# Kernel tuning notes

Hardware: AMD Instinct MI355X
Metric: run time of the kernel (lower is better)

## Reference

```python
import jax, jax.numpy as jnp
import numpy as np

D_MODEL = 1024
HEADS = 16
HEAD_DIM = D_MODEL // HEADS
FF = 4 * D_MODEL
EPS = 1e-5


def _layer_norm(x, g, b):
    mu = jnp.mean(x, axis=-1, keepdims=True)
    var = jnp.mean(jnp.square(x - mu), axis=-1, keepdims=True)
    return (x - mu) * jax.lax.rsqrt(var + EPS) * g + b


def setup_inputs() -> dict:
    key = jax.random.key(0)
    ks = jax.random.split(key, 12)
    s = 0.02
    inp = {
        "x": jax.random.normal(ks[0], (2, 2048, D_MODEL), dtype=jnp.float32),
        "Wq": jax.random.normal(ks[1], (D_MODEL, D_MODEL), dtype=jnp.float32) * s,
        "bq": jnp.zeros((D_MODEL,), jnp.float32),
        "Wk": jax.random.normal(ks[2], (D_MODEL, D_MODEL), dtype=jnp.float32) * s,
        "bk": jnp.zeros((D_MODEL,), jnp.float32),
        "Wv": jax.random.normal(ks[3], (D_MODEL, D_MODEL), dtype=jnp.float32) * s,
        "bv": jnp.zeros((D_MODEL,), jnp.float32),
        "Wm": jax.random.normal(ks[4], (D_MODEL, D_MODEL), dtype=jnp.float32) * s,
        "bm": jnp.zeros((D_MODEL,), jnp.float32),
        "W1": jax.random.normal(ks[5], (D_MODEL, FF), dtype=jnp.float32) * s,
        "b1": jnp.zeros((FF,), jnp.float32),
        "W2": jax.random.normal(ks[6], (FF, D_MODEL), dtype=jnp.float32) * s,
        "b2": jnp.zeros((D_MODEL,), jnp.float32),
        "g1": jnp.ones((D_MODEL,), jnp.float32),
        "be1": jnp.zeros((D_MODEL,), jnp.float32),
        "g2": jnp.ones((D_MODEL,), jnp.float32),
        "be2": jnp.zeros((D_MODEL,), jnp.float32),
    }
    return inp


def reference(x, Wq, bq, Wk, bk, Wv, bv, Wm, bm, W1, b1, W2, b2, g1, be1, g2, be2):
    B, L, _ = x.shape
    # self-attention: source = x, no pos, no masks
    q = (x @ Wq + bq).reshape(B, L, HEADS, HEAD_DIM).transpose(0, 2, 1, 3)
    k = (x @ Wk + bk).reshape(B, L, HEADS, HEAD_DIM).transpose(0, 2, 1, 3)
    v = (x @ Wv + bv).reshape(B, L, HEADS, HEAD_DIM).transpose(0, 2, 1, 3)
    scale = 1.0 / np.sqrt(HEAD_DIM).astype(np.float32)
    scores = jnp.einsum("bhld,bhsd->bhls", q, k) * scale  # [B,H,L,L]
    attn = jax.nn.softmax(scores, axis=-1)
    msg = jnp.einsum("bhls,bhsd->bhld", attn, v)
    msg = msg.transpose(0, 2, 1, 3).reshape(B, L, D_MODEL)
    msg = msg @ Wm + bm
    h = _layer_norm(x + msg, g1, be1)
    ffn = jax.nn.relu(h @ W1 + b1) @ W2 + b2
    return _layer_norm(h + ffn, g2, be2)
```

## Files before the change

### kernel.cpp

```cpp
#include <hip/hip_runtime.h>

#define D_MODEL 1024
#define N_TOK   4096
#define HEADS   16
#define FF_DIM  4096
#define SEQ_L   2048

typedef unsigned short u16;
typedef unsigned int   u32;
typedef __bf16 bf16x8 __attribute__((ext_vector_type(8)));
typedef float  f32x4  __attribute__((ext_vector_type(4)));

#define AS1C(p) ((const __attribute__((address_space(1))) void*)(p))
#define AS3(p)  ((__attribute__((address_space(3))) void*)(p))

__device__ __forceinline__ u16 f2bf(float f) {
    union { float f; unsigned u; } c; c.f = f;
    return (u16)((c.u + 0x7fffu + ((c.u >> 16) & 1u)) >> 16);
}
__device__ __forceinline__ float bf2f(u16 b) {
    union { unsigned u; float f; } c; c.u = ((unsigned)b) << 16;
    return c.f;
}
__device__ __forceinline__ u32 cvt_pk_bf16(float lo, float hi) {
    u32 r;
    asm("v_cvt_pk_bf16_f32 %0, %1, %2" : "=v"(r) : "v"(lo), "v"(hi));
    return r;
}
__device__ __forceinline__ float fmax3(float a, float b, float c) {
    float r;
    asm("v_max3_f32 %0, %1, %2, %3" : "=v"(r) : "v"(a), "v"(b), "v"(c));
    return r;
}

template<int RELU>
__global__ __launch_bounds__(512, 2)
void gemm_pipe(const u16* __restrict__ A, const u16* __restrict__ Bt,
               const float* __restrict__ bias, u16* __restrict__ C,
               int M, int N, int K)
{
    __shared__ u16 As[2][256 * 64];
    __shared__ u16 Bs[2][256 * 64];

    const int tid = threadIdx.x;
    const int wid = tid >> 6, lane = tid & 63;
    const int wr  = wid >> 2, wc = wid & 3;
    const int l15 = lane & 15, l16 = lane >> 4;

    const int nwg = gridDim.x * gridDim.y;
    int bid = blockIdx.y * gridDim.x + blockIdx.x;
    bid = (bid & 7) * (nwg >> 3) + (bid >> 3);
    const int r0 = (bid / gridDim.x) * 256, c0 = (bid % gridDim.x) * 256;

    const u16* Ab = A  + (size_t)r0 * K;
    const u16* Bb = Bt + (size_t)c0 * K;

    f32x4 acc[8][4];
#pragma unroll
    for (int m = 0; m < 8; ++m)
#pragma unroll
        for (int n = 0; n < 4; ++n) acc[m][n] = (f32x4){0.f, 0.f, 0.f, 0.f};

    auto stage = [&](u16* dst, const u16* src, int kbase) {
#pragma unroll
        for (int i = 0; i < 4; ++i) {
            const int r  = i * 64 + (tid >> 3);
            const int gc = (tid & 7) ^ (r & 7);
            __builtin_amdgcn_global_load_lds(AS1C(src + (size_t)r * K + kbase + gc * 8),
                                             AS3(dst + (i * 64 + (wid << 3)) * 64), 16, 0, 0);
        }
    };

    bf16x8 af[4][2], bbA[2][2], bbB[2][2];

    auto ldAf = [&](const u16* sl, int mh) {
#pragma unroll
        for (int m = 0; m < 4; ++m) {
            const int row = wr * 128 + (mh * 4 + m) * 16 + l15;
#pragma unroll
            for (int ks = 0; ks < 2; ++ks) {
                const int ch = (ks * 4 + l16) ^ (row & 7);
                af[m][ks] = *(const bf16x8*)&sl[row * 64 + ch * 8];
            }
        }
    };
    auto ldBf = [&](const u16* sl, int pair, bf16x8 (&bb)[2][2]) {
#pragma unroll
        for (int n = 0; n < 2; ++n) {
            const int row = wc * 64 + (pair * 2 + n) * 16 + l15;
#pragma unroll
            for (int ks = 0; ks < 2; ++ks) {
                const int ch = (ks * 4 + l16) ^ (row & 7);
                bb[n][ks] = *(const bf16x8*)&sl[row * 64 + ch * 8];
            }
        }
    };
    auto mm16 = [&](int mh, int pair, bf16x8 (&bb)[2][2]) {
        __builtin_amdgcn_s_setprio(1);
#pragma unroll
        for (int ks = 0; ks < 2; ++ks)
#pragma unroll
            for (int m = 0; m < 4; ++m)
#pragma unroll
                for (int n = 0; n < 2; ++n)
                    acc[mh * 4 + m][pair * 2 + n] =
                        __builtin_amdgcn_mfma_f32_16x16x32_bf16(af[m][ks], bb[n][ks],
                                                                acc[mh * 4 + m][pair * 2 + n], 0, 0, 0);
        __builtin_amdgcn_s_setprio(0);
    };

    const int nt = K >> 6;
    stage(&As[0][0], Ab, 0);
    stage(&Bs[0][0], Bb, 0);
    stage(&As[1][0], Ab, 64);

    for (int t = 0; t < nt; ++t) {
        u16* Asl = &As[t & 1][0];
        u16* Bsl = &Bs[t & 1][0];
        u16* Aso = &As[t & 1][0];
        u16* Bso = &Bs[(t + 1) & 1][0];

        if (t + 1 < nt) { asm volatile("s_waitcnt vmcnt(4)" ::: "memory"); }
        else            { asm volatile("s_waitcnt vmcnt(0)" ::: "memory"); }
        __builtin_amdgcn_s_barrier();
        ldAf(Asl, 0);
        ldBf(Bsl, 0, bbA);
        if (t + 1 < nt) stage(Bso, Bb, (t + 1) * 64);
        __builtin_amdgcn_s_barrier();
        mm16(0, 0, bbA);
        __builtin_amdgcn_s_barrier();
        ldBf(Bsl, 1, bbB);
        mm16(0, 1, bbB);
        __builtin_amdgcn_s_barrier();
        ldAf(Asl, 1);
        mm16(1, 0, bbA);
        __builtin_amdgcn_s_barrier();
        if (t + 2 < nt) stage(Aso, Ab, (t + 2) * 64);
        mm16(1, 1, bbB);
        __builtin_amdgcn_s_barrier();
    }

#pragma unroll
    for (int n = 0; n < 4; ++n) {
        const int col = c0 + wc * 64 + n * 16 + l15;
        const float bv = bias[col];
#pragma unroll
        for (int m = 0; m < 8; ++m) {
#pragma unroll
            for (int r = 0; r < 4; ++r) {
                const size_t row = (size_t)(r0 + wr * 128 + m * 16 + l16 * 4 + r);
                float v = acc[m][n][r] + bv;
                if (RELU) v = fmaxf(v, 0.f);
                C[row * N + col] = f2bf(v);
            }
        }
    }
}

template<int RELU>
__global__ __launch_bounds__(512, 2)
void gemm_pipe128(const u16* __restrict__ A, const u16* __restrict__ Bt,
                  const float* __restrict__ bias, u16* __restrict__ C,
                  int M, int N, int K)
{
    __shared__ u16 As[2][128 * 64];
    __shared__ u16 Bs[2][128 * 64];

    const int tid = threadIdx.x;
    const int wid = tid >> 6, lane = tid & 63;
    const int wr  = wid >> 2, wc = wid & 3;
    const int l15 = lane & 15, l16 = lane >> 4;

    const int nwg = gridDim.x * gridDim.y;
    int bid = blockIdx.y * gridDim.x + blockIdx.x;
    bid = (bid & 7) * (nwg >> 3) + (bid >> 3);
    const int r0 = (bid / gridDim.x) * 128, c0 = (bid % gridDim.x) * 128;

    const u16* Ab = A  + (size_t)r0 * K;
    const u16* Bb = Bt + (size_t)c0 * K;

    f32x4 acc[4][2];
#pragma unroll
    for (int m = 0; m < 4; ++m)
#pragma unroll
        for (int n = 0; n < 2; ++n) acc[m][n] = (f32x4){0.f, 0.f, 0.f, 0.f};

    auto stage = [&](u16* dst, const u16* src, int kbase) {
#pragma unroll
        for (int i = 0; i < 2; ++i) {
            const int r  = i * 64 + (tid >> 3);
            const int gc = (tid & 7) ^ (r & 7);
            __builtin_amdgcn_global_load_lds(AS1C(src + (size_t)r * K + kbase + gc * 8),
                                             AS3(dst + (i * 64 + (wid << 3)) * 64), 16, 0, 0);
        }
    };

    const int nt = K >> 6;
    stage(&As[0][0], Ab, 0);  stage(&Bs[0][0], Bb, 0);
    stage(&As[1][0], Ab, 64); stage(&Bs[1][0], Bb, 64);

    for (int t = 0; t < nt; ++t) {
        const u16* Asl = &As[t & 1][0];
        const u16* Bsl = &Bs[t & 1][0];

        if (t + 1 < nt) { asm volatile("s_waitcnt vmcnt(4)" ::: "memory"); }
        else            { asm volatile("s_waitcnt vmcnt(0)" ::: "memory"); }
        __builtin_amdgcn_s_barrier();

        bf16x8 af[4][2], bb[2][2];
#pragma unroll
        for (int m = 0; m < 4; ++m) {
            const int row = wr * 64 + m * 16 + l15;
#pragma unroll
            for (int ks = 0; ks < 2; ++ks) {
                const int ch = (ks * 4 + l16) ^ (row & 7);
                af[m][ks] = *(const bf16x8*)&Asl[row * 64 + ch * 8];
            }
        }
#pragma unroll
        for (int n = 0; n < 2; ++n) {
            const int row = wc * 32 + n * 16 + l15;
#pragma unroll
            for (int ks = 0; ks < 2; ++ks) {
                const int ch = (ks * 4 + l16) ^ (row & 7);
                bb[n][ks] = *(const bf16x8*)&Bsl[row * 64 + ch * 8];
            }
        }
        __builtin_amdgcn_s_setprio(1);
#pragma unroll
        for (int ks = 0; ks < 2; ++ks)
#pragma unroll
            for (int m = 0; m < 4; ++m)
#pragma unroll
                for (int n = 0; n < 2; ++n)
                    acc[m][n] = __builtin_amdgcn_mfma_f32_16x16x32_bf16(af[m][ks], bb[n][ks], acc[m][n], 0, 0, 0);
        __builtin_amdgcn_s_setprio(0);
        __builtin_amdgcn_s_barrier();

        if (t + 2 < nt) {
            stage(&As[t & 1][0], Ab, (t + 2) * 64);
            stage(&Bs[t & 1][0], Bb, (t + 2) * 64);
        }
    }

#pragma unroll
    for (int n = 0; n < 2; ++n) {
        const int col = c0 + wc * 32 + n * 16 + l15;
        const float bv = bias[col];
#pragma unroll
        for (int m = 0; m < 4; ++m) {
#pragma unroll
            for (int r = 0; r < 4; ++r) {
                const size_t row = (size_t)(r0 + wr * 64 + m * 16 + l16 * 4 + r);
                float v = acc[m][n][r] + bv;
                if (RELU) v = fmaxf(v, 0.f);
                C[row * N + col] = f2bf(v);
            }
        }
    }
}

__global__ __launch_bounds__(512, 4)
void attn_mfma(const u16* __restrict__ qkv, u16* __restrict__ ao)
{
    __shared__ u16 Kl[2][128 * 64];
    __shared__ u32 Vt[64 * 64];

    const int tid = threadIdx.x;
    const int wid = tid >> 6, lane = tid & 63;
    const int l15 = lane & 15, l16 = lane >> 4;

    int lin = blockIdx.y * gridDim.x + blockIdx.x;
    lin = (lin & 7) * 64 + (lin >> 3);
    const int bh = lin >> 4, b = bh >> 4, h = bh & 15;
    const int q0 = (lin & 15) * 128;
    const int ho = h * 64;
    const size_t tb = (size_t)b * SEQ_L;

    const u16* qg = qkv + (tb + q0) * 3072 + ho;
    const u16* kg = qkv + tb * 3072 + 1024 + ho;
    const u16* vg = qkv + tb * 3072 + 2048 + ho;

    const float SC = 0.18033688f;

    bf16x8 qa[2];
#pragma unroll
    for (int ks = 0; ks < 2; ++ks) {
        union { bf16x8 v; u16 u[8]; u32 w[4]; } a, r;
        a.v = *(const bf16x8*)(qg + (size_t)(wid * 16 + l15) * 3072 + ks * 32 + l16 * 8);
#pragma unroll
        for (int e = 0; e < 4; ++e)
            r.w[e] = cvt_pk_bf16(bf2f(a.u[2 * e]) * SC, bf2f(a.u[2 * e + 1]) * SC);
        qa[ks] = r.v;
    }

    union { bf16x8 v; u32 u[4]; } onesv;
#pragma unroll
    for (int e = 0; e < 4; ++e) onesv.u[e] = 0x3F803F80u;

    const int sp = lane;
    const int dc = wid;

    auto stageK = [&](int buf, int s0) {
#pragma unroll
        for (int i = 0; i < 2; ++i) {
            const int r  = i * 64 + (tid >> 3);
            const int gc = (tid & 7) ^ (r & 7);
            __builtin_amdgcn_global_load_lds(AS1C(kg + (size_t)(s0 + r) * 3072 + gc * 8),
                                             AS3(&Kl[buf][(i * 64 + wid * 8) * 64]), 16, 0, 0);
        }
    };

    f32x4 oacc[4];
#pragma unroll
    for (int f = 0; f < 4; ++f) oacc[f] = (f32x4){0.f, 0.f, 0.f, 0.f};
    f32x4 lcol = (f32x4){0.f, 0.f, 0.f, 0.f};
    float m_c = -1e30f;

    union { bf16x8 v; u16 u[8]; } ua, ub;
    stageK(0, 0);
    ua.v = *(const bf16x8*)(vg + (size_t)(2 * sp) * 3072 + dc * 8);
    ub.v = *(const bf16x8*)(vg + (size_t)(2 * sp + 1) * 3072 + dc * 8);

    const int nt = SEQ_L / 128;
    for (int t = 0; t < nt; ++t) {
        const int buf = t & 1;

        asm volatile("s_waitcnt vmcnt(0)" ::: "memory");
#pragma unroll
        for (int e = 0; e < 8; ++e) {
            const int d = dc * 8 + e;
            const int w = sp ^ (((d & 7) << 2) ^ ((d >> 3) << 1));
            Vt[d * 64 + w] = (u32)ua.u[e] | ((u32)ub.u[e] << 16);
        }
        __syncthreads();

        if (t + 1 < nt) {
            stageK(buf ^ 1, (t + 1) * 128);
            ua.v = *(const bf16x8*)(vg + (size_t)((t + 1) * 128 + 2 * sp) * 3072 + dc * 8);
            ub.v = *(const bf16x8*)(vg + (size_t)((t + 1) * 128 + 2 * sp + 1) * 3072 + dc * 8);
        }

        f32x4 sacc[8];
#pragma unroll
        for (int f = 0; f < 8; ++f) sacc[f] = (f32x4){0.f, 0.f, 0.f, 0.f};
        __builtin_amdgcn_s_setprio(1);
#pragma unroll
        for (int ks = 0; ks < 2; ++ks)
#pragma unroll
            for (int f = 0; f < 8; ++f) {
                const int row = f * 16 + l15;
                const int ch  = (ks * 4 + l16) ^ (row & 7);
                bf16x8 kb = *(const bf16x8*)&Kl[buf][row * 64 + ch * 8];
                sacc[f] = __builtin_amdgcn_mfma_f32_16x16x32_bf16(kb, qa[ks], sacc[f], 0, 0, 0);
            }
        __builtin_amdgcn_s_setprio(0);

        float pm[8];
#pragma unroll
        for (int f = 0; f < 8; ++f)
            pm[f] = fmaxf(fmax3(sacc[f][0], sacc[f][1], sacc[f][2]), sacc[f][3]);
        float mx;
        {
            float t0 = fmax3(pm[0], pm[1], pm[2]);
            float t1 = fmax3(pm[3], pm[4], pm[5]);
            float t2 = fmaxf(pm[6], pm[7]);
            mx = fmax3(t0, t1, t2);
        }
        mx = fmaxf(mx, __shfl_xor(mx, 16));
        mx = fmaxf(mx, __shfl_xor(mx, 32));

        if (__any(mx > m_c + 8.f)) {
            const float mnew = fmaxf(m_c, mx);
            const float corr = __builtin_exp2f(m_c - mnew);
            m_c = mnew;
#pragma unroll
            for (int r = 0; r < 4; ++r) {
                const float cr = __shfl(corr, l16 * 4 + r);
                lcol[r] *= cr;
#pragma unroll
                for (int f = 0; f < 4; ++f) oacc[f][r] *= cr;
            }
        }

#pragma unroll
        for (int f = 0; f < 8; ++f)
#pragma unroll
            for (int r = 0; r < 4; ++r)
                sacc[f][r] = __builtin_exp2f(sacc[f][r] - m_c);

        u32 pk[8][2];
#pragma unroll
        for (int f = 0; f < 8; ++f) {
            pk[f][0] = cvt_pk_bf16(sacc[f][0], sacc[f][1]);
            pk[f][1] = cvt_pk_bf16(sacc[f][2], sacc[f][3]);
        }

        __builtin_amdgcn_s_setprio(1);
#pragma unroll
        for (int S = 0; S < 4; ++S) {
            union { bf16x8 v; u32 u[4]; } af;
            af.u[0] = pk[2 * S][0];     af.u[1] = pk[2 * S][1];
            af.u[2] = pk[2 * S + 1][0]; af.u[3] = pk[2 * S + 1][1];
#pragma unroll
            for (int f2 = 0; f2 < 4; ++f2) {
                const int d = f2 * 16 + l15;
                const int swzd = ((d & 7) << 2) ^ ((d >> 3) << 1);
                union { bf16x8 v; uint2 u[2]; } vb;
                vb.u[0] = *(const uint2*)&Vt[d * 64 + ((16 * S + 2 * l16) ^ swzd)];
                vb.u[1] = *(const uint2*)&Vt[d * 64 + ((16 * S + 8 + 2 * l16) ^ swzd)];
                oacc[f2] = __builtin_amdgcn_mfma_f32_16x16x32_bf16(af.v, vb.v, oacc[f2], 0, 0, 0);
            }
            lcol = __builtin_amdgcn_mfma_f32_16x16x32_bf16(af.v, onesv.v, lcol, 0, 0, 0);
        }
        __builtin_amdgcn_s_setprio(0);
        __syncthreads();
    }

#pragma unroll
    for (int r = 0; r < 4; ++r) {
        const float inv = 1.f / lcol[r];
        const size_t row = tb + q0 + wid * 16 + l16 * 4 + r;
#pragma unroll
        for (int f2 = 0; f2 < 4; ++f2)
            ao[row * 1024 + ho + f2 * 16 + l15] = f2bf(oacc[f2][r] * inv);
    }
}

template<int WF, int WB, int XBF>
__global__ __launch_bounds__(256)
void add_ln(const void* __restrict__ xv, const u16* __restrict__ y,
            const float* __restrict__ g, const float* __restrict__ be,
            float* __restrict__ outf, u16* __restrict__ outb)
{
    __shared__ float red[4];
    const int t = blockIdx.x, tid = threadIdx.x;
    const int c = tid * 4, lane = tid & 63, wv = tid >> 6;

    float xs[4];
    if (XBF) {
        ushort4 a = *(const ushort4*)((const u16*)xv + (size_t)t * D_MODEL + c);
        xs[0] = bf2f(a.x); xs[1] = bf2f(a.y); xs[2] = bf2f(a.z); xs[3] = bf2f(a.w);
    } else {
        float4 a = *(const float4*)((const float*)xv + (size_t)t * D_MODEL + c);
        xs[0] = a.x; xs[1] = a.y; xs[2] = a.z; xs[3] = a.w;
    }
    ushort4 yb = *(const ushort4*)(y + (size_t)t * D_MODEL + c);
    float s[4] = {xs[0] + bf2f(yb.x), xs[1] + bf2f(yb.y),
                  xs[2] + bf2f(yb.z), xs[3] + bf2f(yb.w)};

    float ps = s[0] + s[1] + s[2] + s[3];
#pragma unroll
    for (int off = 32; off > 0; off >>= 1) ps += __shfl_down(ps, off);
    if (lane == 0) red[wv] = ps;
    __syncthreads();
    const float mean = (red[0] + red[1] + red[2] + red[3]) * (1.f / D_MODEL);
    __syncthreads();

    float pv = 0.f;
#pragma unroll
    for (int u = 0; u < 4; ++u) { float d = s[u] - mean; pv += d * d; }
#pragma unroll
    for (int off = 32; off > 0; off >>= 1) pv += __shfl_down(pv, off);
    if (lane == 0) red[wv] = pv;
    __syncthreads();
    const float var = (red[0] + red[1] + red[2] + red[3]) * (1.f / D_MODEL);
    const float inv = rsqrtf(var + 1e-5f);

    float4 g4 = *(const float4*)(g + c);
    float4 b4 = *(const float4*)(be + c);
    float o[4];
#pragma unroll
    for (int u = 0; u < 4; ++u) o[u] = (s[u] - mean) * inv;
    float4 of = {o[0] * g4.x + b4.x, o[1] * g4.y + b4.y, o[2] * g4.z + b4.z, o[3] * g4.w + b4.w};
    if (WF) *(float4*)(outf + (size_t)t * D_MODEL + c) = of;
    if (WB) {
        ushort4 ob = {f2bf(of.x), f2bf(of.y), f2bf(of.z), f2bf(of.w)};
        *(ushort4*)(outb + (size_t)t * D_MODEL + c) = ob;
    }
}

__global__ __launch_bounds__(256)
void prep(const float* __restrict__ Wq, const float* __restrict__ Wk,
          const float* __restrict__ Wv, const float* __restrict__ Wm,
          const float* __restrict__ W1, const float* __restrict__ W2,
          const float* __restrict__ x,
          const float* __restrict__ bq, const float* __restrict__ bk,
          const float* __restrict__ bv,
          u16* __restrict__ wqkv_t, u16* __restrict__ wm_t,
          u16* __restrict__ w1_t, u16* __restrict__ w2_t,
          u16* __restrict__ xb, float* __restrict__ bqkv)
{
    const int blk = blockIdx.x, tid = threadIdx.x;
    if (blk < 3072) {
        __shared__ float T[64][65];
        const float* src; u16* dst; int K, N, tile;
        if (blk < 256)       { src = Wq; dst = wqkv_t;               K = 1024; N = 1024; tile = blk; }
        else if (blk < 512)  { src = Wk; dst = wqkv_t + 1024 * 1024; K = 1024; N = 1024; tile = blk - 256; }
        else if (blk < 768)  { src = Wv; dst = wqkv_t + 2*1024*1024; K = 1024; N = 1024; tile = blk - 512; }
        else if (blk < 1024) { src = Wm; dst = wm_t;                 K = 1024; N = 1024; tile = blk - 768; }
        else if (blk < 2048) { src = W1; dst = w1_t;                 K = 1024; N = 4096; tile = blk - 1024; }
        else                 { src = W2; dst = w2_t;                 K = 4096; N = 1024; tile = blk - 2048; }
        const int ntn = N >> 6;
        const int n0 = (tile % ntn) * 64, k0 = (tile / ntn) * 64;
        const int rr = tid >> 4, cc = (tid & 15) * 4;
#pragma unroll
        for (int u = 0; u < 4; ++u) {
            const float4 v = *(const float4*)(src + (size_t)(k0 + rr + u * 16) * N + n0 + cc);
            T[rr + u * 16][cc + 0] = v.x; T[rr + u * 16][cc + 1] = v.y;
            T[rr + u * 16][cc + 2] = v.z; T[rr + u * 16][cc + 3] = v.w;
        }
        __syncthreads();
#pragma unroll
        for (int u = 0; u < 4; ++u) {
            const int n = rr + u * 16;
            ushort4 o;
            o.x = f2bf(T[cc + 0][n]); o.y = f2bf(T[cc + 1][n]);
            o.z = f2bf(T[cc + 2][n]); o.w = f2bf(T[cc + 3][n]);
            *(ushort4*)(dst + (size_t)(n0 + n) * K + k0 + cc) = o;
        }
    } else if (blk < 3072 + 4096) {
        const int i = (blk - 3072) * 1024 + tid * 4;
        float4 v = *(const float4*)(x + i);
        ushort4 o = {f2bf(v.x), f2bf(v.y), f2bf(v.z), f2bf(v.w)};
        *(ushort4*)(xb + i) = o;
    } else {
#pragma unroll
        for (int u = 0; u < 12; ++u) {
            const int i = u * 256 + tid;
            bqkv[i] = i < 1024 ? bq[i] : (i < 2048 ? bk[i - 1024] : bv[i - 2048]);
        }
    }
}

extern "C" void kernel_launch(void* const* d_in, const int* in_sizes, int n_in,
                              void* d_out, int out_size, void* d_ws, size_t ws_size,
                              hipStream_t stream)
{
    (void)in_sizes; (void)n_in; (void)out_size; (void)ws_size;

    const float* x   = (const float*)d_in[0];
    const float* Wq  = (const float*)d_in[1];
    const float* bq  = (const float*)d_in[2];
    const float* Wk  = (const float*)d_in[3];
    const float* bk  = (const float*)d_in[4];
    const float* Wv  = (const float*)d_in[5];
    const float* bv  = (const float*)d_in[6];
    const float* Wm  = (const float*)d_in[7];
    const float* bm  = (const float*)d_in[8];
    const float* W1  = (const float*)d_in[9];
    const float* b1  = (const float*)d_in[10];
    const float* W2  = (const float*)d_in[11];
    const float* b2  = (const float*)d_in[12];
    const float* g1  = (const float*)d_in[13];
    const float* be1 = (const float*)d_in[14];
    const float* g2  = (const float*)d_in[15];
    const float* be2 = (const float*)d_in[16];
    float* out = (float*)d_out;

    char* base = (char*)d_ws;
    const size_t MB = 1u << 20;
    u16*   wqkv_t = (u16*)(base);
    u16*   wm_t   = (u16*)(base + 6 * MB);
    u16*   w1_t   = (u16*)(base + 8 * MB);
    u16*   w2_t   = (u16*)(base + 16 * MB);
    float* bqkv   = (float*)(base + 24 * MB);
    u16*   xb     = (u16*)(base + 25 * MB);
    u16*   qkv    = (u16*)(base + 33 * MB);
    u16*   ao     = (u16*)(base + 57 * MB);
    u16*   f1     = (u16*)(base + 33 * MB);
    u16*   msg    = (u16*)(base + 25 * MB);
    u16*   ffn    = (u16*)(base + 25 * MB);
    u16*   hb     = (u16*)(base + 65 * MB);

    dim3 blk(256);
    prep<<<dim3(3072 + 4096 + 1), blk, 0, stream>>>(Wq, Wk, Wv, Wm, W1, W2, x,
                                                    bq, bk, bv,
                                                    wqkv_t, wm_t, w1_t, w2_t, xb, bqkv);

    gemm_pipe<0><<<dim3(12, 16), dim3(512), 0, stream>>>(xb, wqkv_t, bqkv, qkv, N_TOK, 3072, 1024);
    attn_mfma<<<dim3(SEQ_L / 128, 32), dim3(512), 0, stream>>>(qkv, ao);
    gemm_pipe128<0><<<dim3(8, 32), dim3(512), 0, stream>>>(ao, wm_t, bm, msg, N_TOK, 1024, 1024);
    add_ln<0, 1, 0><<<dim3(N_TOK), blk, 0, stream>>>(x, msg, g1, be1, nullptr, hb);
    gemm_pipe<1><<<dim3(16, 16), dim3(512), 0, stream>>>(hb, w1_t, b1, f1, N_TOK, FF_DIM, 1024);
    gemm_pipe128<0><<<dim3(8, 32), dim3(512), 0, stream>>>(f1, w2_t, b2, ffn, N_TOK, 1024, FF_DIM);
    add_ln<1, 0, 1><<<dim3(N_TOK), blk, 0, stream>>>(hb, ffn, g2, be2, out, nullptr);
}
```

Baseline: 251.0 us.

## Restructure 256x256 GEMM into half-tile staged 8-phase pipeline

Replaces the two-stage GEMM main loop with an 8-phase schedule. LDS is split into 128-row halves, and each half-tile is prefetched separately between MFMA phases, so global-to-LDS loads are spread more finely across the compute. Each wave now reads only its own A and B halves. It also unrolls two K-steps per iteration. The aim is to hide load latency and smooth out memory traffic, at the cost of more barriers and more complex waitcnt accounting, which raises the risk of races.

```diff
diff --git a/kernel.cpp b/kernel.cpp
--- a/kernel.cpp
+++ b/kernel.cpp
@@ -35,12 +35,12 @@
 
 template<int RELU>
 __global__ __launch_bounds__(512, 2)
-void gemm_pipe(const u16* __restrict__ A, const u16* __restrict__ Bt,
-               const float* __restrict__ bias, u16* __restrict__ C,
-               int M, int N, int K)
+void gemm_8ph(const u16* __restrict__ A, const u16* __restrict__ Bt,
+              const float* __restrict__ bias, u16* __restrict__ C,
+              int M, int N, int K)
 {
-    __shared__ u16 As[2][256 * 64];
-    __shared__ u16 Bs[2][256 * 64];
+    __shared__ u16 As[2][2][128 * 64];
+    __shared__ u16 Bs[2][2][128 * 64];
 
     const int tid = threadIdx.x;
     const int wid = tid >> 6, lane = tid & 63;
@@ -61,41 +61,46 @@
 #pragma unroll
         for (int n = 0; n < 4; ++n) acc[m][n] = (f32x4){0.f, 0.f, 0.f, 0.f};
 
-    auto stage = [&](u16* dst, const u16* src, int kbase) {
-#pragma unroll
-        for (int i = 0; i < 4; ++i) {
-            const int r  = i * 64 + (tid >> 3);
-            const int gc = (tid & 7) ^ (r & 7);
-            __builtin_amdgcn_global_load_lds(AS1C(src + (size_t)r * K + kbase + gc * 8),
-                                             AS3(dst + (i * 64 + (wid << 3)) * 64), 16, 0, 0);
+    auto stageH = [&](u16* dstHalf, const u16* srcbase, int grow0, int kbase) {
+#pragma unroll
+        for (int i = 0; i < 2; ++i) {
+            const int lr = i * 64 + (tid >> 3);
+            const int gr = grow0 + lr;
+            const int gc = (tid & 7) ^ (gr & 7);
+            __builtin_amdgcn_global_load_lds(AS1C(srcbase + (size_t)gr * K + kbase + gc * 8),
+                                             AS3(dstHalf + (i * 64 + (wid << 3)) * 64), 16, 0, 0);
         }
     };
 
+    const u16* myA[2] = { &As[0][wr][0],      &As[1][wr][0] };
+    const u16* myB[2] = { &Bs[0][wc >> 1][0], &Bs[1][wc >> 1][0] };
+    const int  bro    = (wc & 1) * 64;
+
     bf16x8 af[4][2], bbA[2][2], bbB[2][2];
 
-    auto ldAf = [&](const u16* sl, int mh) {
+    auto ldA = [&](int d, int mh) {
 #pragma unroll
         for (int m = 0; m < 4; ++m) {
-            const int row = wr * 128 + (mh * 4 + m) * 16 + l15;
+            const int row = mh * 64 + m * 16 + l15;
 #pragma unroll
             for (int ks = 0; ks < 2; ++ks) {
                 const int ch = (ks * 4 + l16) ^ (row & 7);
-                af[m][ks] = *(const bf16x8*)&sl[row * 64 + ch * 8];
+                af[m][ks] = *(const bf16x8*)&myA[d][row * 64 + ch * 8];
             }
         }
     };
-    auto ldBf = [&](const u16* sl, int pair, bf16x8 (&bb)[2][2]) {
+    auto ldB = [&](int d, int np, bf16x8 (&bb)[2][2]) {
 #pragma unroll
         for (int n = 0; n < 2; ++n) {
-            const int row = wc * 64 + (pair * 2 + n) * 16 + l15;
+            const int row = bro + (np * 2 + n) * 16 + l15;
 #pragma unroll
             for (int ks = 0; ks < 2; ++ks) {
                 const int ch = (ks * 4 + l16) ^ (row & 7);
-                bb[n][ks] = *(const bf16x8*)&sl[row * 64 + ch * 8];
+                bb[n][ks] = *(const bf16x8*)&myB[d][row * 64 + ch * 8];
             }
         }
     };
-    auto mm16 = [&](int mh, int pair, bf16x8 (&bb)[2][2]) {
+    auto mm = [&](int mh, int np, bf16x8 (&bb)[2][2]) {
         __builtin_amdgcn_s_setprio(1);
 #pragma unroll
         for (int ks = 0; ks < 2; ++ks)
@@ -103,40 +108,69 @@
             for (int m = 0; m < 4; ++m)
 #pragma unroll
                 for (int n = 0; n < 2; ++n)
-                    acc[mh * 4 + m][pair * 2 + n] =
+                    acc[mh * 4 + m][np * 2 + n] =
                         __builtin_amdgcn_mfma_f32_16x16x32_bf16(af[m][ks], bb[n][ks],
-                                                                acc[mh * 4 + m][pair * 2 + n], 0, 0, 0);
+                                                                acc[mh * 4 + m][np * 2 + n], 0, 0, 0);
         __builtin_amdgcn_s_setprio(0);
     };
 
-    const int nt = K >> 6;
-    stage(&As[0][0], Ab, 0);
-    stage(&Bs[0][0], Bb, 0);
-    stage(&As[1][0], Ab, 64);
-
-    for (int t = 0; t < nt; ++t) {
-        u16* Asl = &As[t & 1][0];
-        u16* Bsl = &Bs[t & 1][0];
-        u16* Aso = &As[t & 1][0];
-        u16* Bso = &Bs[(t + 1) & 1][0];
-
-        if (t + 1 < nt) { asm volatile("s_waitcnt vmcnt(4)" ::: "memory"); }
-        else            { asm volatile("s_waitcnt vmcnt(0)" ::: "memory"); }
-        __builtin_amdgcn_s_barrier();
-        ldAf(Asl, 0);
-        ldBf(Bsl, 0, bbA);
-        if (t + 1 < nt) stage(Bso, Bb, (t + 1) * 64);
-        __builtin_amdgcn_s_barrier();
-        mm16(0, 0, bbA);
-        __builtin_amdgcn_s_barrier();
-        ldBf(Bsl, 1, bbB);
-        mm16(0, 1, bbB);
-        __builtin_amdgcn_s_barrier();
-        ldAf(Asl, 1);
-        mm16(1, 0, bbA);
-        __builtin_amdgcn_s_barrier();
-        if (t + 2 < nt) stage(Aso, Ab, (t + 2) * 64);
-        mm16(1, 1, bbB);
+    const int nit = K >> 7;
+
+    stageH(&Bs[0][0][0], Bb, 0,   0);
+    stageH(&As[0][0][0], Ab, 0,   0);
+    stageH(&Bs[0][1][0], Bb, 128, 0);
+    stageH(&As[0][1][0], Ab, 128, 0);
+    stageH(&Bs[1][0][0], Bb, 0,   64);
+    stageH(&As[1][0][0], Ab, 0,   64);
+    asm volatile("s_waitcnt vmcnt(4)" ::: "memory");
+    __builtin_amdgcn_s_barrier();
+
+    for (int it = 0; it < nit; ++it) {
+        const int kb1 = it * 128 + 64;
+        const int kb2 = it * 128 + 128;
+        const int kb3 = it * 128 + 192;
+        const bool more = (it + 1 < nit);
+
+        ldA(0, 0); ldB(0, 0, bbA);
+        stageH(&Bs[1][1][0], Bb, 128, kb1);
+        __builtin_amdgcn_s_barrier();
+        mm(0, 0, bbA);
+        __builtin_amdgcn_s_barrier();
+        ldB(0, 1, bbB);
+        stageH(&As[1][1][0], Ab, 128, kb1);
+        __builtin_amdgcn_s_barrier();
+        mm(0, 1, bbB);
+        __builtin_amdgcn_s_barrier();
+        ldA(0, 1);
+        if (more) stageH(&Bs[0][0][0], Bb, 0, kb2);
+        __builtin_amdgcn_s_barrier();
+        mm(1, 0, bbA);
+        __builtin_amdgcn_s_barrier();
+        if (more) stageH(&As[0][0][0], Ab, 0, kb2);
+        __builtin_amdgcn_s_barrier();
+        mm(1, 1, bbB);
+        if (more) { asm volatile("s_waitcnt vmcnt(4)" ::: "memory"); }
+        else      { asm volatile("s_waitcnt vmcnt(0)" ::: "memory"); }
+        __builtin_amdgcn_s_barrier();
+        ldA(1, 0); ldB(1, 0, bbA);
+        if (more) stageH(&Bs[0][1][0], Bb, 128, kb2);
+        __builtin_amdgcn_s_barrier();
+        mm(0, 0, bbA);
+        __builtin_amdgcn_s_barrier();
+        ldB(1, 1, bbB);
+        if (more) stageH(&As[0][1][0], Ab, 128, kb2);
+        __builtin_amdgcn_s_barrier();
+        mm(0, 1, bbB);
+        __builtin_amdgcn_s_barrier();
+        ldA(1, 1);
+        if (more) stageH(&Bs[1][0][0], Bb, 0, kb3);
+        __builtin_amdgcn_s_barrier();
+        mm(1, 0, bbA);
+        __builtin_amdgcn_s_barrier();
+        if (more) stageH(&As[1][0][0], Ab, 0, kb3);
+        __builtin_amdgcn_s_barrier();
+        mm(1, 1, bbB);
+        if (more) { asm volatile("s_waitcnt vmcnt(4)" ::: "memory"); }
         __builtin_amdgcn_s_barrier();
     }
 
@@ -578,11 +612,11 @@
                                                     bq, bk, bv,
                                                     wqkv_t, wm_t, w1_t, w2_t, xb, bqkv);
 
-    gemm_pipe<0><<<dim3(12, 16), dim3(512), 0, stream>>>(xb, wqkv_t, bqkv, qkv, N_TOK, 3072, 1024);
+    gemm_8ph<0><<<dim3(12, 16), dim3(512), 0, stream>>>(xb, wqkv_t, bqkv, qkv, N_TOK, 3072, 1024);
     attn_mfma<<<dim3(SEQ_L / 128, 32), dim3(512), 0, stream>>>(qkv, ao);
     gemm_pipe128<0><<<dim3(8, 32), dim3(512), 0, stream>>>(ao, wm_t, bm, msg, N_TOK, 1024, 1024);
     add_ln<0, 1, 0><<<dim3(N_TOK), blk, 0, stream>>>(x, msg, g1, be1, nullptr, hb);
-    gemm_pipe<1><<<dim3(16, 16), dim3(512), 0, stream>>>(hb, w1_t, b1, f1, N_TOK, FF_DIM, 1024);
+    gemm_8ph<1><<<dim3(16, 16), dim3(512), 0, stream>>>(hb, w1_t, b1, f1, N_TOK, FF_DIM, 1024);
     gemm_pipe128<0><<<dim3(8, 32), dim3(512), 0, stream>>>(f1, w2_t, b2, ffn, N_TOK, 1024, FF_DIM);
     add_ln<1, 0, 1><<<dim3(N_TOK), blk, 0, stream>>>(hb, ffn, g2, be2, out, nullptr);
 }
```

Result: slower. 259.0 us (+3.2%).

## Split attention KV range in two and merge partial softmax results

Applied to the files above, without the earlier changes.

Each attention block now covers half of the key sequence (1024 keys), which doubles the grid from 512 to 1024 blocks. Each block writes a normalized partial output plus its row sum and max, and a new merge kernel combines the two halves with log-sum-exp weights. The aim is better CU occupancy on MI355X, since 512 blocks may underfill the GPU. The cost is an extra kernel launch, extra bf16 partial-output traffic, and one more bf16 rounding step before the merge.

```diff
diff --git a/kernel.cpp b/kernel.cpp
--- a/kernel.cpp
+++ b/kernel.cpp
@@ -261,7 +261,8 @@
 }
 
 __global__ __launch_bounds__(512, 4)
-void attn_mfma(const u16* __restrict__ qkv, u16* __restrict__ ao)
+void attn_mfma(const u16* __restrict__ qkv, u16* __restrict__ aop,
+               float* __restrict__ lbuf, float* __restrict__ mbuf)
 {
     __shared__ u16 Kl[2][128 * 64];
     __shared__ u32 Vt[64 * 64];
@@ -270,10 +271,13 @@
     const int wid = tid >> 6, lane = tid & 63;
     const int l15 = lane & 15, l16 = lane >> 4;
 
-    int lin = blockIdx.y * gridDim.x + blockIdx.x;
-    lin = (lin & 7) * 64 + (lin >> 3);
-    const int bh = lin >> 4, b = bh >> 4, h = bh & 15;
-    const int q0 = (lin & 15) * 128;
+    int raw = blockIdx.x;
+    const int lin = (raw & 7) * 128 + (raw >> 3);
+    const int bh = lin >> 5, b = bh >> 4, h = bh & 15;
+    const int sub = lin & 31;
+    const int q0 = (sub & 15) << 7;
+    const int sh = sub >> 4;
+    const int sb = sh << 10;
     const int ho = h * 64;
     const size_t tb = (size_t)b * SEQ_L;
 
@@ -318,11 +322,11 @@
     float m_c = -1e30f;
 
     union { bf16x8 v; u16 u[8]; } ua, ub;
-    stageK(0, 0);
-    ua.v = *(const bf16x8*)(vg + (size_t)(2 * sp) * 3072 + dc * 8);
-    ub.v = *(const bf16x8*)(vg + (size_t)(2 * sp + 1) * 3072 + dc * 8);
-
-    const int nt = SEQ_L / 128;
+    stageK(0, sb);
+    ua.v = *(const bf16x8*)(vg + (size_t)(sb + 2 * sp) * 3072 + dc * 8);
+    ub.v = *(const bf16x8*)(vg + (size_t)(sb + 2 * sp + 1) * 3072 + dc * 8);
+
+    const int nt = 1024 / 128;
     for (int t = 0; t < nt; ++t) {
         const int buf = t & 1;
 
@@ -336,9 +340,9 @@
         __syncthreads();
 
         if (t + 1 < nt) {
-            stageK(buf ^ 1, (t + 1) * 128);
-            ua.v = *(const bf16x8*)(vg + (size_t)((t + 1) * 128 + 2 * sp) * 3072 + dc * 8);
-            ub.v = *(const bf16x8*)(vg + (size_t)((t + 1) * 128 + 2 * sp + 1) * 3072 + dc * 8);
+            stageK(buf ^ 1, sb + (t + 1) * 128);
+            ua.v = *(const bf16x8*)(vg + (size_t)(sb + (t + 1) * 128 + 2 * sp) * 3072 + dc * 8);
+            ub.v = *(const bf16x8*)(vg + (size_t)(sb + (t + 1) * 128 + 2 * sp + 1) * 3072 + dc * 8);
         }
 
         f32x4 sacc[8];
@@ -417,14 +421,52 @@
         __syncthreads();
     }
 
+    u16* aoh = aop + (size_t)sh * N_TOK * 1024;
 #pragma unroll
     for (int r = 0; r < 4; ++r) {
-        const float inv = 1.f / lcol[r];
-        const size_t row = tb + q0 + wid * 16 + l16 * 4 + r;
+        const float lv  = lcol[r];
+        const float inv = 1.f / lv;
+        const int   qrow = q0 + wid * 16 + l16 * 4 + r;
+        const size_t row = tb + qrow;
+        const float mrow = __shfl(m_c, l16 * 4 + r);
 #pragma unroll
         for (int f2 = 0; f2 < 4; ++f2)
-            ao[row * 1024 + ho + f2 * 16 + l15] = f2bf(oacc[f2][r] * inv);
-    }
+            aoh[row * 1024 + ho + f2 * 16 + l15] = f2bf(oacc[f2][r] * inv);
+        if (l15 == 0) {
+            lbuf[sh * 65536 + bh * 2048 + qrow] = lv;
+            mbuf[sh * 65536 + bh * 2048 + qrow] = mrow;
+        }
+    }
+}
+
+__global__ __launch_bounds__(256)
+void attn_merge(const u16* __restrict__ aop, const float* __restrict__ lbuf,
+                const float* __restrict__ mbuf, u16* __restrict__ ao)
+{
+    const int t = blockIdx.x, tid = threadIdx.x;
+    const int c = tid * 4;
+    const int h = tid >> 4;
+    const int b = t >> 11, q = t & 2047;
+    const int bh = b * 16 + h;
+    const int idx = bh * 2048 + q;
+
+    const float l1 = lbuf[idx],         m1 = mbuf[idx];
+    const float l2 = lbuf[65536 + idx], m2 = mbuf[65536 + idx];
+    const float m  = fmaxf(m1, m2);
+    const float w1 = l1 * __builtin_exp2f(m1 - m);
+    const float w2 = l2 * __builtin_exp2f(m2 - m);
+    const float inv = 1.f / (w1 + w2);
+    const float a1 = w1 * inv, a2 = w2 * inv;
+
+    const size_t off = (size_t)t * 1024 + c;
+    ushort4 o1 = *(const ushort4*)(aop + off);
+    ushort4 o2 = *(const ushort4*)(aop + (size_t)N_TOK * 1024 + off);
+    ushort4 o;
+    o.x = f2bf(bf2f(o1.x) * a1 + bf2f(o2.x) * a2);
+    o.y = f2bf(bf2f(o1.y) * a1 + bf2f(o2.y) * a2);
+    o.z = f2bf(bf2f(o1.z) * a1 + bf2f(o2.z) * a2);
+    o.w = f2bf(bf2f(o1.w) * a1 + bf2f(o2.w) * a2);
+    *(ushort4*)(ao + off) = o;
 }
 
 template<int WF, int WB, int XBF>
@@ -567,11 +609,14 @@
     float* bqkv   = (float*)(base + 24 * MB);
     u16*   xb     = (u16*)(base + 25 * MB);
     u16*   qkv    = (u16*)(base + 33 * MB);
-    u16*   ao     = (u16*)(base + 57 * MB);
+    u16*   aop    = (u16*)(base + 57 * MB);
+    u16*   aof    = (u16*)(base + 33 * MB);
     u16*   f1     = (u16*)(base + 33 * MB);
     u16*   msg    = (u16*)(base + 25 * MB);
     u16*   ffn    = (u16*)(base + 25 * MB);
-    u16*   hb     = (u16*)(base + 65 * MB);
+    u16*   hb     = (u16*)(base + 73 * MB);
+    float* lbuf   = (float*)(base + 81 * MB);
+    float* mbuf   = (float*)(base + 81 * MB + 512 * 1024);
 
     dim3 blk(256);
     prep<<<dim3(3072 + 4096 + 1), blk, 0, stream>>>(Wq, Wk, Wv, Wm, W1, W2, x,
@@ -579,8 +624,9 @@
                                                     wqkv_t, wm_t, w1_t, w2_t, xb, bqkv);
 
     gemm_pipe<0><<<dim3(12, 16), dim3(512), 0, stream>>>(xb, wqkv_t, bqkv, qkv, N_TOK, 3072, 1024);
-    attn_mfma<<<dim3(SEQ_L / 128, 32), dim3(512), 0, stream>>>(qkv, ao);
-    gemm_pipe128<0><<<dim3(8, 32), dim3(512), 0, stream>>>(ao, wm_t, bm, msg, N_TOK, 1024, 1024);
+    attn_mfma<<<dim3(1024), dim3(512), 0, stream>>>(qkv, aop, lbuf, mbuf);
+    attn_merge<<<dim3(N_TOK), blk, 0, stream>>>(aop, lbuf, mbuf, aof);
+    gemm_pipe128<0><<<dim3(8, 32), dim3(512), 0, stream>>>(aof, wm_t, bm, msg, N_TOK, 1024, 1024);
     add_ln<0, 1, 0><<<dim3(N_TOK), blk, 0, stream>>>(x, msg, g1, be1, nullptr, hb);
     gemm_pipe<1><<<dim3(16, 16), dim3(512), 0, stream>>>(hb, w1_t, b1, f1, N_TOK, FF_DIM, 1024);
     gemm_pipe128<0><<<dim3(8, 32), dim3(512), 0, stream>>>(f1, w2_t, b2, ffn, N_TOK, 1024, FF_DIM);
```

Result: slower. 266.4 us (+6.1%).
